# Performance work log

Hardware: AMD Instinct MI355X
Metric: run time of the kernel (lower is better)

The kernel has to match this reference:

```python
import jax, jax.numpy as jnp
import numpy as np

B, N, M = 8192, 4096, 4096  # batch tokens, input_size, output_size


def setup_inputs() -> dict:
    key = jax.random.key(0)
    k1, k2, k3, k4, k5 = jax.random.split(key, 5)
    x = jax.random.normal(k1, (B, N), dtype=jnp.float32)
    W_m = jax.random.normal(k2, (N, M), dtype=jnp.float32) * 0.001
    W_u = jnp.full((N,), np.log(0.01), dtype=jnp.float32) + 0.01 * jax.random.normal(k3, (N,), dtype=jnp.float32)
    W_v = jnp.full((M,), np.log(0.01), dtype=jnp.float32) + 0.01 * jax.random.normal(k4, (M,), dtype=jnp.float32)
    eps = jax.random.normal(k5, (N, M), dtype=jnp.float32)
    return {"x": x, "W_m": W_m, "W_u": W_u, "W_v": W_v, "eps": eps}


def reference(x, W_m, W_u, W_v, eps):
    # diag(exp(0.5*u)) @ eps @ diag(exp(0.5*v)) == row/col elementwise scaling
    W = W_m + jnp.exp(0.5 * W_u)[:, None] * eps * jnp.exp(0.5 * W_v)[None, :]
    return x @ W  # [B, M]; original forward never adds bias
```

## Files before the change

### kernel.cpp

```cpp
#include <hip/hip_runtime.h>
#include <hip/hip_bf16.h>

typedef short bf16x8 __attribute__((ext_vector_type(8)));
typedef short short8 __attribute__((ext_vector_type(8)));
typedef float f32x4  __attribute__((ext_vector_type(4)));

__device__ __forceinline__ short f2bf(float f) {
    union { float f; unsigned u; } a; a.f = f;
    unsigned r = a.u + 0x7fffu + ((a.u >> 16) & 1u);
    return (short)(r >> 16);
}

__device__ __forceinline__ void gload16(const void* g, void* l) {
    __builtin_amdgcn_global_load_lds(
        (const __attribute__((address_space(1))) unsigned int*)g,
        (__attribute__((address_space(3))) unsigned int*)l,
        16, 0, 0);
}

__global__ __launch_bounds__(256) void cvt_x(const float* __restrict__ x,
                                             short* __restrict__ xb, long n) {
    const long t = (long)blockIdx.x * blockDim.x + threadIdx.x;
    const long stride = (long)gridDim.x * blockDim.x;
    for (long i = t * 8; i < n; i += stride * 8) {
        float4 v0 = *(const float4*)&x[i];
        float4 v1 = *(const float4*)&x[i + 4];
        short8 o;
        o[0] = f2bf(v0.x); o[1] = f2bf(v0.y); o[2] = f2bf(v0.z); o[3] = f2bf(v0.w);
        o[4] = f2bf(v1.x); o[5] = f2bf(v1.y); o[6] = f2bf(v1.z); o[7] = f2bf(v1.w);
        *(short8*)&xb[i] = o;
    }
}

__global__ __launch_bounds__(256) void build_wt(const float* __restrict__ Wm,
                                                const float* __restrict__ eps,
                                                const float* __restrict__ Wu,
                                                const float* __restrict__ Wv,
                                                short* __restrict__ Wt,
                                                int N, int M) {
    __shared__ __align__(16) short tile[64][68];
    __shared__ float su[64], sv[64];
    const int n0 = blockIdx.y * 64, m0 = blockIdx.x * 64;
    const int t = threadIdx.x;
    if (t < 64)        su[t]      = __expf(0.5f * Wu[n0 + t]);
    else if (t < 128)  sv[t - 64] = __expf(0.5f * Wv[m0 + t - 64]);
    __syncthreads();
    for (int c = t; c < 1024; c += 256) {
        const int row = c >> 4, c4 = c & 15;
        const long g = (long)(n0 + row) * M + m0 + c4 * 4;
        float4 wm = *(const float4*)&Wm[g];
        float4 ep = *(const float4*)&eps[g];
        const float s = su[row];
        short4 o;
        o.x = f2bf(wm.x + s * ep.x * sv[c4 * 4 + 0]);
        o.y = f2bf(wm.y + s * ep.y * sv[c4 * 4 + 1]);
        o.z = f2bf(wm.z + s * ep.z * sv[c4 * 4 + 2]);
        o.w = f2bf(wm.w + s * ep.w * sv[c4 * 4 + 3]);
        *(short4*)&tile[row][c4 * 4] = o;
    }
    __syncthreads();
    for (int c = t; c < 512; c += 256) {
        const int mm = c >> 3, nn8 = (c & 7) * 8;
        bf16x8 o;
        #pragma unroll
        for (int j = 0; j < 8; ++j) o[j] = tile[nn8 + j][mm];
        *(bf16x8*)&Wt[(long)(m0 + mm) * N + n0 + nn8] = o;
    }
}

#define KDIM 4096

template<int BUF, int MH>
__device__ __forceinline__ void load_a(const char* sm, int aoff, int c0, int c1,
                                       bf16x8 (&a)[4][2]) {
    const char* pa = sm + BUF * 32768 + MH * 16384 + aoff;
    #pragma unroll
    for (int mf = 0; mf < 4; ++mf) {
        a[mf][0] = *(const bf16x8*)(pa + mf * 2048 + c0);
        a[mf][1] = *(const bf16x8*)(pa + mf * 2048 + c1);
    }
}

template<int BUF, int NH>
__device__ __forceinline__ void load_b(const char* sm, int boff, int c0, int c1,
                                       bf16x8 (&b)[2][2]) {
    const char* pb = sm + 65536 + BUF * 32768 + NH * 16384 + boff;
    #pragma unroll
    for (int nf = 0; nf < 2; ++nf) {
        b[nf][0] = *(const bf16x8*)(pb + nf * 2048 + c0);
        b[nf][1] = *(const bf16x8*)(pb + nf * 2048 + c1);
    }
}

template<int MH, int NH>
__device__ __forceinline__ void do_mfma(const bf16x8 (&a)[4][2], const bf16x8 (&b)[2][2],
                                        f32x4 (&acc)[8][4]) {
    #pragma unroll
    for (int mf = 0; mf < 4; ++mf)
        #pragma unroll
        for (int nf = 0; nf < 2; ++nf)
            #pragma unroll
            for (int ks = 0; ks < 2; ++ks)
                acc[MH * 4 + mf][NH * 2 + nf] = __builtin_amdgcn_mfma_f32_16x16x32_bf16(
                    a[mf][ks], b[nf][ks], acc[MH * 4 + mf][NH * 2 + nf], 0, 0, 0);
}

__device__ __forceinline__ void stage2(const short* g, char* l) {
    gload16(g, l);
    gload16(g + 8 * KDIM, l + 1024);
}

__global__ __launch_bounds__(512, 2) void gemm256(const short* __restrict__ A,
                                                  const short* __restrict__ Bt,
                                                  float* __restrict__ C) {
    __shared__ __align__(16) char smem[131072];
    const char* smc = smem;

    const int tid = threadIdx.x;
    const int wid = tid >> 6, lane = tid & 63;
    const int wm = wid >> 2, wn = wid & 3;
    const int l15 = lane & 15, l4 = lane >> 4;

    const int bsw = (blockIdx.x & 7) * 64 + (blockIdx.x >> 3);
    const int bx = bsw & 15, by = bsw >> 4;
    const int brow = by * 256, bcol = bx * 256;

    const int s7 = l15 & 7;
    const int c0 = ((l4) ^ s7) * 16;
    const int c1 = ((l4 + 4) ^ s7) * 16;
    const int aoff = (wm * 64 + l15) * 128;
    const int boff = (wn * 32 + l15) * 128;

    const int p0 = wid * 128 + lane;
    const int srow = p0 >> 3;
    const int sk = (p0 & 7) ^ (srow & 7);
    const short* gA = A  + (long)(brow + srow) * KDIM + sk * 8;
    const short* gB = Bt + (long)(bcol + srow) * KDIM + sk * 8;
    char* smw = smem + wid * 2048;

#define STAGE_A(BUF, H, T) stage2(gA + (H) * (128 * KDIM) + (T) * 64, smw + (BUF) * 32768 + (H) * 16384)
#define STAGE_B(BUF, H, T) stage2(gB + (H) * (128 * KDIM) + (T) * 64, smw + 65536 + (BUF) * 32768 + (H) * 16384)
#define BAR   __builtin_amdgcn_s_barrier()
#define LGKM0 asm volatile("s_waitcnt lgkmcnt(0)")
#define LGKM8 asm volatile("s_waitcnt lgkmcnt(8)")
#define VM4   asm volatile("s_waitcnt vmcnt(4)" ::: "memory")
#define PRIO1 __builtin_amdgcn_s_setprio(1)
#define PRIO0 __builtin_amdgcn_s_setprio(0)

    f32x4 acc[8][4];
    #pragma unroll
    for (int i = 0; i < 8; ++i)
        #pragma unroll
        for (int j = 0; j < 4; ++j) acc[i][j] = {0.f, 0.f, 0.f, 0.f};

    STAGE_A(0, 0, 0);
    STAGE_B(0, 0, 0);
    STAGE_B(0, 1, 0);
    STAGE_A(0, 1, 0);
    STAGE_A(1, 0, 1);
    STAGE_B(1, 0, 1);
    asm volatile("s_waitcnt vmcnt(4)" ::: "memory");
    BAR;

    bf16x8 Afr[4][2], B0fr[2][2], B1fr[2][2];

    for (int it = 0; it < 32; ++it) {
        const int T = 2 * it;
        const int t1 = T + 1;
        const int t2 = (T + 2) & 63;
        const int t3 = (T + 3) & 63;

        load_a<0, 0>(smc, aoff, c0, c1, Afr);
        load_b<0, 0>(smc, boff, c0, c1, B0fr);
        STAGE_B(1, 1, t1);
        LGKM8; BAR; LGKM0;
        PRIO1; do_mfma<0, 0>(Afr, B0fr, acc); PRIO0;
        BAR;
        load_b<0, 1>(smc, boff, c0, c1, B1fr);
        STAGE_A(1, 1, t1);
        BAR; LGKM0;
        PRIO1; do_mfma<0, 1>(Afr, B1fr, acc); PRIO0;
        BAR;
        load_a<0, 1>(smc, aoff, c0, c1, Afr);
        STAGE_A(0, 0, t2);
        BAR; LGKM0;
        PRIO1; do_mfma<1, 1>(Afr, B1fr, acc); PRIO0;
        BAR;
        STAGE_B(0, 0, t2);
        VM4; BAR;
        PRIO1; do_mfma<1, 0>(Afr, B0fr, acc); PRIO0;
        BAR;

        load_a<1, 0>(smc, aoff, c0, c1, Afr);
        load_b<1, 0>(smc, boff, c0, c1, B0fr);
        STAGE_B(0, 1, t2);
        LGKM8; BAR; LGKM0;
        PRIO1; do_mfma<0, 0>(Afr, B0fr, acc); PRIO0;
        BAR;
        load_b<1, 1>(smc, boff, c0, c1, B1fr);
        STAGE_A(0, 1, t2);
        BAR; LGKM0;
        PRIO1; do_mfma<0, 1>(Afr, B1fr, acc); PRIO0;
        BAR;
        load_a<1, 1>(smc, aoff, c0, c1, Afr);
        STAGE_A(1, 0, t3);
        BAR; LGKM0;
        PRIO1; do_mfma<1, 1>(Afr, B1fr, acc); PRIO0;
        BAR;
        STAGE_B(1, 0, t3);
        VM4; BAR;
        PRIO1; do_mfma<1, 0>(Afr, B0fr, acc); PRIO0;
        BAR;
    }

    const int cr = l4 * 4;
    #pragma unroll
    for (int mh = 0; mh < 2; ++mh)
        #pragma unroll
        for (int mf = 0; mf < 4; ++mf) {
            const long row = brow + mh * 128 + wm * 64 + mf * 16 + cr;
            #pragma unroll
            for (int nh = 0; nh < 2; ++nh)
                #pragma unroll
                for (int nf = 0; nf < 2; ++nf) {
                    const long col = bcol + nh * 128 + wn * 32 + nf * 16 + l15;
                    const f32x4 v = acc[mh * 4 + mf][nh * 2 + nf];
                    float* p = C + row * 4096 + col;
                    p[0]        = v[0];
                    p[4096]     = v[1];
                    p[2 * 4096] = v[2];
                    p[3 * 4096] = v[3];
                }
        }
#undef STAGE_A
#undef STAGE_B
#undef BAR
#undef LGKM0
#undef LGKM8
#undef VM4
#undef PRIO1
#undef PRIO0
}

extern "C" void kernel_launch(void* const* d_in, const int* in_sizes, int n_in,
                              void* d_out, int out_size, void* d_ws, size_t ws_size,
                              hipStream_t stream) {
    const float* x   = (const float*)d_in[0];
    const float* Wm  = (const float*)d_in[1];
    const float* Wu  = (const float*)d_in[2];
    const float* Wv  = (const float*)d_in[3];
    const float* eps = (const float*)d_in[4];
    float* out = (float*)d_out;

    const int N = in_sizes[2];
    const int M = in_sizes[3];
    const int B = in_sizes[0] / N;

    short* xb = (short*)d_ws;
    short* wt = (short*)((char*)d_ws + (size_t)B * N * 2);

    cvt_x<<<2048, 256, 0, stream>>>(x, xb, (long)B * N);
    build_wt<<<dim3(M / 64, N / 64), 256, 0, stream>>>(Wm, eps, Wu, Wv, wt, N, M);
    gemm256<<<dim3((B / 256) * (M / 256)), 512, 0, stream>>>(xb, wt, out);
}
```

Before: 537.3 us.

## Restructure GEMM software pipeline to prefetch a full tile ahead and double-buffer B fragments

Reorders the global-to-LDS staging so a whole K-tile (both halves of A and B) is issued ahead, with a vmcnt(6) wait in the prologue. Adds a second register buffer for the B0 fragment so the next tile's B0 can be read from LDS during the current tile's last MFMA phase, removing the combined A+B LDS load at the start of each half-iteration. The aim is to hide LDS and global latency behind MFMA work, at the cost of extra registers and a more fragile wait-count scheme.

```diff
diff --git a/kernel.cpp b/kernel.cpp
--- a/kernel.cpp
+++ b/kernel.cpp
@@ -142,8 +142,8 @@
 #define STAGE_B(BUF, H, T) stage2(gB + (H) * (128 * KDIM) + (T) * 64, smw + 65536 + (BUF) * 32768 + (H) * 16384)
 #define BAR   __builtin_amdgcn_s_barrier()
 #define LGKM0 asm volatile("s_waitcnt lgkmcnt(0)")
-#define LGKM8 asm volatile("s_waitcnt lgkmcnt(8)")
 #define VM4   asm volatile("s_waitcnt vmcnt(4)" ::: "memory")
+#define VM6   asm volatile("s_waitcnt vmcnt(6)" ::: "memory")
 #define PRIO1 __builtin_amdgcn_s_setprio(1)
 #define PRIO0 __builtin_amdgcn_s_setprio(0)
 
@@ -153,63 +153,65 @@
         #pragma unroll
         for (int j = 0; j < 4; ++j) acc[i][j] = {0.f, 0.f, 0.f, 0.f};
 
+    STAGE_B(0, 0, 0);
     STAGE_A(0, 0, 0);
-    STAGE_B(0, 0, 0);
     STAGE_B(0, 1, 0);
     STAGE_A(0, 1, 0);
+    STAGE_B(1, 0, 1);
     STAGE_A(1, 0, 1);
-    STAGE_B(1, 0, 1);
-    asm volatile("s_waitcnt vmcnt(4)" ::: "memory");
+    STAGE_B(1, 1, 1);
+    STAGE_A(1, 1, 1);
+    VM6;
     BAR;
 
-    bf16x8 Afr[4][2], B0fr[2][2], B1fr[2][2];
+    bf16x8 Afr[4][2], B0a[2][2], B0b[2][2], B1fr[2][2];
+    load_b<0, 0>(smc, boff, c0, c1, B0a);
 
     for (int it = 0; it < 32; ++it) {
         const int T = 2 * it;
-        const int t1 = T + 1;
         const int t2 = (T + 2) & 63;
         const int t3 = (T + 3) & 63;
 
         load_a<0, 0>(smc, aoff, c0, c1, Afr);
-        load_b<0, 0>(smc, boff, c0, c1, B0fr);
-        STAGE_B(1, 1, t1);
-        LGKM8; BAR; LGKM0;
-        PRIO1; do_mfma<0, 0>(Afr, B0fr, acc); PRIO0;
+        STAGE_B(0, 0, t2);
+        BAR; LGKM0;
+        PRIO1; do_mfma<0, 0>(Afr, B0a, acc); PRIO0;
         BAR;
         load_b<0, 1>(smc, boff, c0, c1, B1fr);
-        STAGE_A(1, 1, t1);
+        STAGE_A(0, 0, t2);
         BAR; LGKM0;
         PRIO1; do_mfma<0, 1>(Afr, B1fr, acc); PRIO0;
         BAR;
         load_a<0, 1>(smc, aoff, c0, c1, Afr);
-        STAGE_A(0, 0, t2);
+        STAGE_B(0, 1, t2);
         BAR; LGKM0;
         PRIO1; do_mfma<1, 1>(Afr, B1fr, acc); PRIO0;
         BAR;
-        STAGE_B(0, 0, t2);
-        VM4; BAR;
-        PRIO1; do_mfma<1, 0>(Afr, B0fr, acc); PRIO0;
+        load_b<1, 0>(smc, boff, c0, c1, B0b);
+        STAGE_A(0, 1, t2);
+        VM4; BAR; LGKM0;
+        PRIO1; do_mfma<1, 0>(Afr, B0a, acc); PRIO0;
         BAR;
 
         load_a<1, 0>(smc, aoff, c0, c1, Afr);
-        load_b<1, 0>(smc, boff, c0, c1, B0fr);
-        STAGE_B(0, 1, t2);
-        LGKM8; BAR; LGKM0;
-        PRIO1; do_mfma<0, 0>(Afr, B0fr, acc); PRIO0;
+        STAGE_B(1, 0, t3);
+        BAR; LGKM0;
+        PRIO1; do_mfma<0, 0>(Afr, B0b, acc); PRIO0;
         BAR;
         load_b<1, 1>(smc, boff, c0, c1, B1fr);
-        STAGE_A(0, 1, t2);
+        STAGE_A(1, 0, t3);
         BAR; LGKM0;
         PRIO1; do_mfma<0, 1>(Afr, B1fr, acc); PRIO0;
         BAR;
         load_a<1, 1>(smc, aoff, c0, c1, Afr);
-        STAGE_A(1, 0, t3);
+        STAGE_B(1, 1, t3);
         BAR; LGKM0;
         PRIO1; do_mfma<1, 1>(Afr, B1fr, acc); PRIO0;
         BAR;
-        STAGE_B(1, 0, t3);
-        VM4; BAR;
-        PRIO1; do_mfma<1, 0>(Afr, B0fr, acc); PRIO0;
+        load_b<0, 0>(smc, boff, c0, c1, B0a);
+        STAGE_A(1, 1, t3);
+        VM4; BAR; LGKM0;
+        PRIO1; do_mfma<1, 0>(Afr, B0b, acc); PRIO0;
         BAR;
     }
 
@@ -236,8 +238,8 @@
 #undef STAGE_B
 #undef BAR
 #undef LGKM0
-#undef LGKM8
 #undef VM4
+#undef VM6
 #undef PRIO1
 #undef PRIO0
 }
```

Result: faster. 522.8 us (-2.7%).
